# Performance work log

Hardware: AMD Instinct MI355X
Metric: run time of the kernel (lower is better)

## Reference

```python
import jax, jax.numpy as jnp
import numpy as np

SEQ_LEN = 128
EMBED_DIM = 1024
BATCH = 128


def setup_inputs() -> dict:
    key = jax.random.key(0)
    ks = jax.random.split(key, 9)
    d = EMBED_DIM
    s = 0.02
    return {
        "x": jax.random.normal(ks[0], (BATCH, SEQ_LEN * d), dtype=jnp.float32),
        "Wq": jax.random.normal(ks[1], (d, d), dtype=jnp.float32) * s,
        "bq": jax.random.normal(ks[2], (d,), dtype=jnp.float32) * s,
        "Wk": jax.random.normal(ks[3], (d, d), dtype=jnp.float32) * s,
        "bk": jax.random.normal(ks[4], (d,), dtype=jnp.float32) * s,
        "Wv": jax.random.normal(ks[5], (d, d), dtype=jnp.float32) * s,
        "bv": jax.random.normal(ks[6], (d,), dtype=jnp.float32) * s,
        "Wo": jax.random.normal(ks[7], (d, d), dtype=jnp.float32) * s,
        "bo": jax.random.normal(ks[8], (d,), dtype=jnp.float32) * s,
    }


def reference(x, Wq, bq, Wk, bk, Wv, bv, Wo, bo):
    b = x.shape[0]
    d = EMBED_DIM
    xs = x.reshape(b, SEQ_LEN, d)  # [B, S, D]
    # torch Linear: y = x @ W.T + b
    Q = jnp.einsum("bsd,ed->bse", xs, Wq) + bq
    K = jnp.einsum("bsd,ed->bse", xs, Wk) + bk
    V = jnp.einsum("bsd,ed->bse", xs, Wv) + bv
    scores = jnp.einsum("bse,bte->bst", Q, K) / jnp.sqrt(jnp.float32(d))
    weights = jax.nn.softmax(scores, axis=-1)
    attended = jnp.einsum("bst,bte->bse", weights, V)
    out = jnp.einsum("bse,fe->bsf", attended, Wo) + bo
    return out.reshape(b, -1)
```

## Files before the change

kernel.cpp:

```cpp
#include <hip/hip_runtime.h>
#include <hip/hip_bf16.h>

typedef __attribute__((ext_vector_type(8))) __bf16 bf16x8;
typedef __attribute__((ext_vector_type(4))) __bf16 bf16x4;
typedef __attribute__((ext_vector_type(4))) float f32x4;

#define SEQ 128
#define DIM 1024
#define BATCH 128
#define MTOT (BATCH * SEQ)

__device__ __forceinline__ void gload16(const void* g, void* l) {
    __builtin_amdgcn_global_load_lds(
        (const __attribute__((address_space(1))) void*)g,
        (__attribute__((address_space(3))) void*)l, 16, 0, 0);
}

#define BARRIER() do { asm volatile("" ::: "memory"); __builtin_amdgcn_s_barrier(); asm volatile("" ::: "memory"); } while (0)
#define WAITV(N) asm volatile("s_waitcnt vmcnt(" #N ")" ::: "memory")
#define MFMA(a, b, c) __builtin_amdgcn_mfma_f32_16x16x32_bf16(a, b, c, 0, 0, 0)

__global__ void cast_all(const float* __restrict__ x,
                         const float* __restrict__ Wq, const float* __restrict__ Wk,
                         const float* __restrict__ Wv, const float* __restrict__ Wo,
                         __bf16* __restrict__ Xb,
                         __bf16* __restrict__ Wqb, __bf16* __restrict__ Wkb,
                         __bf16* __restrict__ Wvb, __bf16* __restrict__ Wob) {
    const float* src; __bf16* dst; size_t base;
    if (blockIdx.y == 0) {
        src = x; dst = Xb; base = (size_t)blockIdx.x * 2048;
    } else {
        const int j = blockIdx.x;
        if (j >= 2048) return;
        const int w = j >> 9;
        src = (w == 0) ? Wq : (w == 1) ? Wk : (w == 2) ? Wv : Wo;
        dst = (w == 0) ? Wqb : (w == 1) ? Wkb : (w == 2) ? Wvb : Wob;
        base = (size_t)(j & 511) * 2048;
    }
    const size_t i = base + (size_t)threadIdx.x * 8;
    float4 f0 = *reinterpret_cast<const float4*>(src + i);
    float4 f1 = *reinterpret_cast<const float4*>(src + i + 4);
    bf16x8 o;
    o[0] = (__bf16)f0.x; o[1] = (__bf16)f0.y; o[2] = (__bf16)f0.z; o[3] = (__bf16)f0.w;
    o[4] = (__bf16)f1.x; o[5] = (__bf16)f1.y; o[6] = (__bf16)f1.z; o[7] = (__bf16)f1.w;
    *reinterpret_cast<bf16x8*>(dst + i) = o;
}

#define GEMM_TILE_BODY(RB, SB, TS, DOSTAGE, VMSTMT) do { \
    const __bf16* As_ = &lds[RB][wr][0]; \
    const __bf16* Bs_ = &lds[RB][2 + (wc >> 1)][0]; \
    const int bb_ = (wc & 1) * 64; \
    bf16x8 a0 = LDF(As_, 0 * 16 + lr), a1 = LDF(As_, 1 * 16 + lr); \
    bf16x8 a2 = LDF(As_, 2 * 16 + lr), a3 = LDF(As_, 3 * 16 + lr); \
    bf16x8 a4 = LDF(As_, 4 * 16 + lr), a5 = LDF(As_, 5 * 16 + lr); \
    bf16x8 a6 = LDF(As_, 6 * 16 + lr), a7 = LDF(As_, 7 * 16 + lr); \
    bf16x8 b0 = LDF(Bs_, bb_ + 0 * 16 + lr), b1 = LDF(Bs_, bb_ + 1 * 16 + lr); \
    bf16x8 b2 = LDF(Bs_, bb_ + 2 * 16 + lr), b3 = LDF(Bs_, bb_ + 3 * 16 + lr); \
    if (DOSTAGE) { STAGE_A(SB, TS); STAGE_B(SB, TS); } \
    __builtin_amdgcn_s_setprio(1); \
    acc[0][0] = MFMA(a0, b0, acc[0][0]); acc[0][1] = MFMA(a0, b1, acc[0][1]); \
    acc[0][2] = MFMA(a0, b2, acc[0][2]); acc[0][3] = MFMA(a0, b3, acc[0][3]); \
    acc[1][0] = MFMA(a1, b0, acc[1][0]); acc[1][1] = MFMA(a1, b1, acc[1][1]); \
    acc[1][2] = MFMA(a1, b2, acc[1][2]); acc[1][3] = MFMA(a1, b3, acc[1][3]); \
    acc[2][0] = MFMA(a2, b0, acc[2][0]); acc[2][1] = MFMA(a2, b1, acc[2][1]); \
    acc[2][2] = MFMA(a2, b2, acc[2][2]); acc[2][3] = MFMA(a2, b3, acc[2][3]); \
    acc[3][0] = MFMA(a3, b0, acc[3][0]); acc[3][1] = MFMA(a3, b1, acc[3][1]); \
    acc[3][2] = MFMA(a3, b2, acc[3][2]); acc[3][3] = MFMA(a3, b3, acc[3][3]); \
    acc[4][0] = MFMA(a4, b0, acc[4][0]); acc[4][1] = MFMA(a4, b1, acc[4][1]); \
    acc[4][2] = MFMA(a4, b2, acc[4][2]); acc[4][3] = MFMA(a4, b3, acc[4][3]); \
    acc[5][0] = MFMA(a5, b0, acc[5][0]); acc[5][1] = MFMA(a5, b1, acc[5][1]); \
    acc[5][2] = MFMA(a5, b2, acc[5][2]); acc[5][3] = MFMA(a5, b3, acc[5][3]); \
    acc[6][0] = MFMA(a6, b0, acc[6][0]); acc[6][1] = MFMA(a6, b1, acc[6][1]); \
    acc[6][2] = MFMA(a6, b2, acc[6][2]); acc[6][3] = MFMA(a6, b3, acc[6][3]); \
    acc[7][0] = MFMA(a7, b0, acc[7][0]); acc[7][1] = MFMA(a7, b1, acc[7][1]); \
    acc[7][2] = MFMA(a7, b2, acc[7][2]); acc[7][3] = MFMA(a7, b3, acc[7][3]); \
    __builtin_amdgcn_s_setprio(0); \
    VMSTMT; \
    BARRIER(); \
} while (0)

#define GEMM_MAIN_LOOP() do { \
    STAGE_A(0, 0); STAGE_B(0, 0); \
    STAGE_A(1, 1); STAGE_B(1, 1); \
    STAGE_A(2, 2); STAGE_B(2, 2); \
    WAITV(8); \
    BARRIER(); \
    for (int it = 0; it < 7; ++it) { \
        const int t = it * 4; \
        GEMM_TILE_BODY(0, 3, t + 3, 1, WAITV(8)); \
        GEMM_TILE_BODY(1, 0, t + 4, 1, WAITV(8)); \
        GEMM_TILE_BODY(2, 1, t + 5, 1, WAITV(8)); \
        GEMM_TILE_BODY(3, 2, t + 6, 1, WAITV(8)); \
    } \
    GEMM_TILE_BODY(0, 3, 31, 1, WAITV(8));    \
    GEMM_TILE_BODY(1, 0, 0, 0, WAITV(4));     \
    GEMM_TILE_BODY(2, 0, 0, 0, WAITV(0));     \
    GEMM_TILE_BODY(3, 0, 0, 0, (void)0);      \
} while (0)

__global__ __launch_bounds__(512, 1) void gemm_qkv3(const __bf16* __restrict__ A,
        const __bf16* __restrict__ Wqb, const __bf16* __restrict__ Wkb, const __bf16* __restrict__ Wvb,
        const float* __restrict__ bq, const float* __restrict__ bk, const float* __restrict__ bv,
        __bf16* __restrict__ Qo, __bf16* __restrict__ Ko, __bf16* __restrict__ Vt) {
    const int K = 1024;
    __shared__ __bf16 lds[4][4][4096];
    const int tid = threadIdx.x, wave = tid >> 6, lane = tid & 63;
    const int wr = wave >> 2, wc = wave & 3;
    const int lr = lane & 15;
    const int lkb = ((lane >> 4) & 3) * 16;
    const unsigned bid = blockIdx.x;
    const unsigned swz = (bid & 7) * 96 + (bid >> 3);
    const int mt = swz / 12, nt = swz % 12;
    const int m0 = mt * 256;
    const int n0row = (nt & 3) * 256;
    const int mid = nt >> 2;
    const __bf16* Wsel = (mid == 0) ? Wqb : (mid == 1) ? Wkb : Wvb;
    const float*  bsel = (mid == 0) ? bq  : (mid == 1) ? bk  : bv;

    const int rloc = wave * 16 + (lane >> 2);
    const int cbs  = ((((lane & 3) << 4) ^ (((lane >> 3) & 3) << 4)) >> 1);
    const __bf16* pA = A + (size_t)(m0 + rloc) * K + cbs;
    const __bf16* pB = Wsel + (size_t)(n0row + rloc) * K + cbs;
    const int wo = wave * 512;

    f32x4 acc[8][4] = {};

#define LDF(SLOT, R) (*reinterpret_cast<const bf16x8*>( \
        reinterpret_cast<const char*>(SLOT) + (R) * 64 + (lkb ^ ((((R) >> 1) & 3) << 4))))
#define STAGE_A(SB, TS) do { gload16(pA + (TS) * 32, &lds[SB][0][wo]); \
                             gload16(pA + (size_t)128 * 1024 + (TS) * 32, &lds[SB][1][wo]); } while (0)
#define STAGE_B(SB, TS) do { gload16(pB + (TS) * 32, &lds[SB][2][wo]); \
                             gload16(pB + (size_t)128 * 1024 + (TS) * 32, &lds[SB][3][wo]); } while (0)

    GEMM_MAIN_LOOP();

    const int rbase = (lane >> 4) * 4;
    #pragma unroll
    for (int ri = 0; ri < 8; ++ri) {
        #pragma unroll
        for (int j = 0; j < 4; ++j) {
            const int gcl = n0row + wc * 64 + j * 16 + lr;
            const float bvv = bsel[gcl];
            const int grb = m0 + wr * 128 + ri * 16 + rbase;
            if (mid < 2) {
                __bf16* C = (mid == 0) ? Qo : Ko;
                #pragma unroll
                for (int r = 0; r < 4; ++r)
                    C[(size_t)(grb + r) * DIM + gcl] = (__bf16)(acc[ri][j][r] + bvv);
            } else {
                const int b = grb >> 7, s = grb & 127;
                bf16x4 v;
                #pragma unroll
                for (int r = 0; r < 4; ++r) v[r] = (__bf16)(acc[ri][j][r] + bvv);
                *reinterpret_cast<bf16x4*>(&Vt[((size_t)b * DIM + gcl) * SEQ + s]) = v;
            }
        }
    }
#undef STAGE_A
#undef STAGE_B
#undef LDF
}

__global__ __launch_bounds__(512, 1) void gemm256o(const __bf16* __restrict__ A,
                                                   const __bf16* __restrict__ W,
                                                   const float* __restrict__ bias,
                                                   float* __restrict__ Cout) {
    const int K = 1024, N = 1024;
    __shared__ __bf16 lds[4][4][4096];
    const int tid = threadIdx.x, wave = tid >> 6, lane = tid & 63;
    const int wr = wave >> 2, wc = wave & 3;
    const int lr = lane & 15;
    const int lkb = ((lane >> 4) & 3) * 16;
    const int bid = blockIdx.x;
    const int swz = (bid & 7) * 32 + (bid >> 3);
    const int m0 = (swz >> 2) * 256, n0 = (swz & 3) * 256;
    const int rloc = wave * 16 + (lane >> 2);
    const int cbs  = ((((lane & 3) << 4) ^ (((lane >> 3) & 3) << 4)) >> 1);
    const __bf16* pA = A + (size_t)(m0 + rloc) * K + cbs;
    const __bf16* pB = W + (size_t)(n0 + rloc) * K + cbs;
    const int wo = wave * 512;

    f32x4 acc[8][4] = {};

#define LDF(SLOT, R) (*reinterpret_cast<const bf16x8*>( \
        reinterpret_cast<const char*>(SLOT) + (R) * 64 + (lkb ^ ((((R) >> 1) & 3) << 4))))
#define STAGE_A(SB, TS) do { gload16(pA + (TS) * 32, &lds[SB][0][wo]); \
                             gload16(pA + (size_t)128 * 1024 + (TS) * 32, &lds[SB][1][wo]); } while (0)
#define STAGE_B(SB, TS) do { gload16(pB + (TS) * 32, &lds[SB][2][wo]); \
                             gload16(pB + (size_t)128 * 1024 + (TS) * 32, &lds[SB][3][wo]); } while (0)

    GEMM_MAIN_LOOP();

    const int rbase = (lane >> 4) * 4;
    #pragma unroll
    for (int ri = 0; ri < 8; ++ri) {
        #pragma unroll
        for (int j = 0; j < 4; ++j) {
            const int gc  = n0 + wc * 64 + j * 16 + lr;
            const float bv = bias[gc];
            const int grb = m0 + wr * 128 + ri * 16 + rbase;
            #pragma unroll
            for (int r = 0; r < 4; ++r)
                Cout[(size_t)(grb + r) * N + gc] = acc[ri][j][r] + bv;
        }
    }
#undef STAGE_A
#undef STAGE_B
#undef LDF
}

__global__ __launch_bounds__(256) void attn_kernel(const __bf16* __restrict__ Q,
                                                   const __bf16* __restrict__ Km,
                                                   const __bf16* __restrict__ Vt,
                                                   __bf16* __restrict__ Ab) {
    __shared__ __align__(16) char smem[40960];
    float  (*Ssh)[132] = (float(*)[132])(smem);
    __bf16 (*Psh)[136] = (__bf16(*)[136])(smem + 16896);

    const int bid = blockIdx.x;
    const int logical = (bid & 7) * 64 + (bid >> 3);
    const int b = logical >> 2, rt = logical & 3;
    const int tid = threadIdx.x, wave = tid >> 6, lane = tid & 63;
    const int lr = lane & 15, lk = (lane >> 4) * 8, rbase = (lane >> 4) * 4;
    const __bf16* Qb = Q  + ((size_t)b * SEQ + rt * 32) * DIM;
    const __bf16* Kb = Km + (size_t)b * SEQ * DIM;
    const __bf16* Vb = Vt + (size_t)b * DIM * SEQ;

    const int csrc = ((lane & 7) * 16) ^ (((lane >> 3) & 7) << 4);

    f32x4 acc[2][2] = {};
    {
        auto stage_kq = [&](int buf, int c) {
            char* Kd = smem + buf * 20480 + wave * 4096;
            char* Qd = smem + buf * 20480 + 16384 + wave * 1024;
            const char* Ks = (const char*)Kb + (size_t)(wave * 32 + (lane >> 3)) * 2048 + c * 128 + csrc;
            #pragma unroll
            for (int q = 0; q < 4; ++q)
                gload16(Ks + (size_t)q * 8 * 2048, Kd + q * 1024);
            const char* Qs = (const char*)Qb + (size_t)(wave * 8 + (lane >> 3)) * 2048 + c * 128 + csrc;
            gload16(Qs, Qd);
        };
        stage_kq(0, 0);
        WAITV(0);
        BARRIER();
        for (int c = 0; c < 16; ++c) {
            const int rb = c & 1;
            if (c < 15) stage_kq(rb ^ 1, c + 1);
            const char* Kl = smem + rb * 20480;
            const char* Ql = Kl + 16384;
            bf16x8 qf[2][2], kf[2][2];
            #pragma unroll
            for (int i = 0; i < 2; ++i)
                #pragma unroll
                for (int ks = 0; ks < 2; ++ks) {
                    const int r = i * 16 + lr;
                    qf[i][ks] = *reinterpret_cast<const bf16x8*>(
                        Ql + r * 128 + ((ks * 64 + (lane >> 4) * 16) ^ ((r & 7) << 4)));
                }
            #pragma unroll
            for (int j = 0; j < 2; ++j)
                #pragma unroll
                for (int ks = 0; ks < 2; ++ks) {
                    const int r = wave * 32 + j * 16 + lr;
                    kf[j][ks] = *reinterpret_cast<const bf16x8*>(
                        Kl + r * 128 + ((ks * 64 + (lane >> 4) * 16) ^ ((r & 7) << 4)));
                }
            __builtin_amdgcn_s_setprio(1);
            #pragma unroll
            for (int i = 0; i < 2; ++i)
                #pragma unroll
                for (int j = 0; j < 2; ++j)
                    #pragma unroll
                    for (int ks = 0; ks < 2; ++ks)
                        acc[i][j] = MFMA(qf[i][ks], kf[j][ks], acc[i][j]);
            __builtin_amdgcn_s_setprio(0);
            WAITV(0);
            BARRIER();
        }
    }
    const float scale = 0.03125f;
    #pragma unroll
    for (int i = 0; i < 2; ++i)
        #pragma unroll
        for (int j = 0; j < 2; ++j)
            #pragma unroll
            for (int r = 0; r < 4; ++r)
                Ssh[i * 16 + rbase + r][wave * 32 + j * 16 + lr] = acc[i][j][r] * scale;
    __syncthreads();

    {
        const int row = tid >> 3;
        const int c0  = (tid & 7) * 16;
        float4 v0 = *reinterpret_cast<const float4*>(&Ssh[row][c0]);
        float4 v1 = *reinterpret_cast<const float4*>(&Ssh[row][c0 + 4]);
        float4 v2 = *reinterpret_cast<const float4*>(&Ssh[row][c0 + 8]);
        float4 v3 = *reinterpret_cast<const float4*>(&Ssh[row][c0 + 12]);
        float e[16] = {v0.x, v0.y, v0.z, v0.w, v1.x, v1.y, v1.z, v1.w,
                       v2.x, v2.y, v2.z, v2.w, v3.x, v3.y, v3.z, v3.w};
        float mx = e[0];
        #pragma unroll
        for (int u = 1; u < 16; ++u) mx = fmaxf(mx, e[u]);
        mx = fmaxf(mx, __shfl_xor(mx, 1));
        mx = fmaxf(mx, __shfl_xor(mx, 2));
        mx = fmaxf(mx, __shfl_xor(mx, 4));
        float s = 0.f;
        #pragma unroll
        for (int u = 0; u < 16; ++u) { e[u] = __expf(e[u] - mx); s += e[u]; }
        s += __shfl_xor(s, 1);
        s += __shfl_xor(s, 2);
        s += __shfl_xor(s, 4);
        const float inv = 1.f / s;
        bf16x8 p0, p1;
        #pragma unroll
        for (int u = 0; u < 8; ++u) { p0[u] = (__bf16)(e[u] * inv); p1[u] = (__bf16)(e[u + 8] * inv); }
        *reinterpret_cast<bf16x8*>(&Psh[row][c0])     = p0;
        *reinterpret_cast<bf16x8*>(&Psh[row][c0 + 8]) = p1;
    }
    __syncthreads();

    bf16x8 pf[2][4];
    #pragma unroll
    for (int i = 0; i < 2; ++i)
        #pragma unroll
        for (int ks = 0; ks < 4; ++ks)
            pf[i][ks] = *reinterpret_cast<const bf16x8*>(&Psh[i * 16 + lr][ks * 32 + lk]);
    __syncthreads();

    __bf16* Ao = Ab + ((size_t)b * SEQ + rt * 32) * DIM;
    {
        auto stage_v = [&](int buf, int c) {
            char* Vd = smem + buf * 16384 + wave * 4096;
            #pragma unroll
            for (int q = 0; q < 4; ++q) {
                const int rowl = wave * 16 + q * 4 + (lane >> 4);
                const char* Vs = (const char*)Vb + (size_t)(c * 64 + rowl) * 256 +
                                 (((lane & 15) * 16) ^ ((rowl & 7) << 4));
                gload16(Vs, Vd + q * 1024);
            }
        };
        stage_v(0, 0);
        WAITV(0);
        BARRIER();
        for (int c = 0; c < 16; ++c) {
            const int rb = c & 1;
            if (c < 15) stage_v(rb ^ 1, c + 1);
            const char* Vl = smem + rb * 16384;
            f32x4 a2[2] = {};
            const int r = wave * 16 + lr;
            #pragma unroll
            for (int ks = 0; ks < 4; ++ks) {
                bf16x8 vf = *reinterpret_cast<const bf16x8*>(
                    Vl + r * 256 + ((ks * 64 + (lane >> 4) * 16) ^ ((r & 7) << 4)));
                a2[0] = MFMA(pf[0][ks], vf, a2[0]);
                a2[1] = MFMA(pf[1][ks], vf, a2[1]);
            }
            const int n0 = c * 64 + wave * 16;
            #pragma unroll
            for (int i = 0; i < 2; ++i)
                #pragma unroll
                for (int rr = 0; rr < 4; ++rr)
                    Ao[(size_t)(i * 16 + rbase + rr) * DIM + n0 + lr] = (__bf16)a2[i][rr];
            WAITV(8);
            BARRIER();
        }
    }
}

extern "C" void kernel_launch(void* const* d_in, const int* in_sizes, int n_in,
                              void* d_out, int out_size, void* d_ws, size_t ws_size,
                              hipStream_t stream) {
    const float* x  = (const float*)d_in[0];
    const float* Wq = (const float*)d_in[1];
    const float* bq = (const float*)d_in[2];
    const float* Wk = (const float*)d_in[3];
    const float* bk = (const float*)d_in[4];
    const float* Wv = (const float*)d_in[5];
    const float* bv = (const float*)d_in[6];
    const float* Wo = (const float*)d_in[7];
    const float* bo = (const float*)d_in[8];

    char* ws = (char*)d_ws;
    const size_t MB = 1024 * 1024;
    __bf16* Xb  = (__bf16*)(ws);
    __bf16* Wqb = (__bf16*)(ws + 32 * MB);
    __bf16* Wkb = (__bf16*)(ws + 34 * MB);
    __bf16* Wvb = (__bf16*)(ws + 36 * MB);
    __bf16* Wob = (__bf16*)(ws + 38 * MB);
    __bf16* Qb  = (__bf16*)(ws + 40 * MB);
    __bf16* Kb  = (__bf16*)(ws + 72 * MB);
    __bf16* Vt  = (__bf16*)(ws + 104 * MB);
    __bf16* Ab  = Xb;

    cast_all<<<dim3(8192, 2), 256, 0, stream>>>(x, Wq, Wk, Wv, Wo, Xb, Wqb, Wkb, Wvb, Wob);

    gemm_qkv3<<<768, 512, 0, stream>>>(Xb, Wqb, Wkb, Wvb, bq, bk, bv, Qb, Kb, Vt);

    attn_kernel<<<512, 256, 0, stream>>>(Qb, Kb, Vt, Ab);

    gemm256o<<<256, 512, 0, stream>>>(Ab, Wob, bo, (float*)d_out);
}
```

Measured before the change: 187.4 us.

## Double-buffer LDS-to-register fragments to overlap LDS reads with MFMA

Restructures the GEMM main loop so the register fragments for the next K-tile are read from LDS while the MFMAs for the current tile run, using two register fragment sets (f0/f1). Global-to-LDS staging is issued at the start of each step, and the vmcnt wait drops from 8 to 4 so the tile being read next is resident. This aims to hide LDS read latency behind matrix math. In exchange it roughly doubles fragment register usage, which could cause spills, and it tightens the wait and barrier ordering around buffer reuse.

```diff
diff --git a/kernel.cpp b/kernel.cpp
--- a/kernel.cpp
+++ b/kernel.cpp
@@ -46,56 +46,63 @@
     *reinterpret_cast<bf16x8*>(dst + i) = o;
 }
 
-#define GEMM_TILE_BODY(RB, SB, TS, DOSTAGE, VMSTMT) do { \
+
+#define RF(P, RB) do { \
     const __bf16* As_ = &lds[RB][wr][0]; \
     const __bf16* Bs_ = &lds[RB][2 + (wc >> 1)][0]; \
     const int bb_ = (wc & 1) * 64; \
-    bf16x8 a0 = LDF(As_, 0 * 16 + lr), a1 = LDF(As_, 1 * 16 + lr); \
-    bf16x8 a2 = LDF(As_, 2 * 16 + lr), a3 = LDF(As_, 3 * 16 + lr); \
-    bf16x8 a4 = LDF(As_, 4 * 16 + lr), a5 = LDF(As_, 5 * 16 + lr); \
-    bf16x8 a6 = LDF(As_, 6 * 16 + lr), a7 = LDF(As_, 7 * 16 + lr); \
-    bf16x8 b0 = LDF(Bs_, bb_ + 0 * 16 + lr), b1 = LDF(Bs_, bb_ + 1 * 16 + lr); \
-    bf16x8 b2 = LDF(Bs_, bb_ + 2 * 16 + lr), b3 = LDF(Bs_, bb_ + 3 * 16 + lr); \
-    if (DOSTAGE) { STAGE_A(SB, TS); STAGE_B(SB, TS); } \
+    P##a0 = LDF(As_, 0 * 16 + lr); P##a1 = LDF(As_, 1 * 16 + lr); \
+    P##a2 = LDF(As_, 2 * 16 + lr); P##a3 = LDF(As_, 3 * 16 + lr); \
+    P##a4 = LDF(As_, 4 * 16 + lr); P##a5 = LDF(As_, 5 * 16 + lr); \
+    P##a6 = LDF(As_, 6 * 16 + lr); P##a7 = LDF(As_, 7 * 16 + lr); \
+    P##b0 = LDF(Bs_, bb_ + 0 * 16 + lr); P##b1 = LDF(Bs_, bb_ + 1 * 16 + lr); \
+    P##b2 = LDF(Bs_, bb_ + 2 * 16 + lr); P##b3 = LDF(Bs_, bb_ + 3 * 16 + lr); \
+} while (0)
+
+#define MM(P) do { \
     __builtin_amdgcn_s_setprio(1); \
-    acc[0][0] = MFMA(a0, b0, acc[0][0]); acc[0][1] = MFMA(a0, b1, acc[0][1]); \
-    acc[0][2] = MFMA(a0, b2, acc[0][2]); acc[0][3] = MFMA(a0, b3, acc[0][3]); \
-    acc[1][0] = MFMA(a1, b0, acc[1][0]); acc[1][1] = MFMA(a1, b1, acc[1][1]); \
-    acc[1][2] = MFMA(a1, b2, acc[1][2]); acc[1][3] = MFMA(a1, b3, acc[1][3]); \
-    acc[2][0] = MFMA(a2, b0, acc[2][0]); acc[2][1] = MFMA(a2, b1, acc[2][1]); \
-    acc[2][2] = MFMA(a2, b2, acc[2][2]); acc[2][3] = MFMA(a2, b3, acc[2][3]); \
-    acc[3][0] = MFMA(a3, b0, acc[3][0]); acc[3][1] = MFMA(a3, b1, acc[3][1]); \
-    acc[3][2] = MFMA(a3, b2, acc[3][2]); acc[3][3] = MFMA(a3, b3, acc[3][3]); \
-    acc[4][0] = MFMA(a4, b0, acc[4][0]); acc[4][1] = MFMA(a4, b1, acc[4][1]); \
-    acc[4][2] = MFMA(a4, b2, acc[4][2]); acc[4][3] = MFMA(a4, b3, acc[4][3]); \
-    acc[5][0] = MFMA(a5, b0, acc[5][0]); acc[5][1] = MFMA(a5, b1, acc[5][1]); \
-    acc[5][2] = MFMA(a5, b2, acc[5][2]); acc[5][3] = MFMA(a5, b3, acc[5][3]); \
-    acc[6][0] = MFMA(a6, b0, acc[6][0]); acc[6][1] = MFMA(a6, b1, acc[6][1]); \
-    acc[6][2] = MFMA(a6, b2, acc[6][2]); acc[6][3] = MFMA(a6, b3, acc[6][3]); \
-    acc[7][0] = MFMA(a7, b0, acc[7][0]); acc[7][1] = MFMA(a7, b1, acc[7][1]); \
-    acc[7][2] = MFMA(a7, b2, acc[7][2]); acc[7][3] = MFMA(a7, b3, acc[7][3]); \
+    acc[0][0] = MFMA(P##a0, P##b0, acc[0][0]); acc[0][1] = MFMA(P##a0, P##b1, acc[0][1]); \
+    acc[0][2] = MFMA(P##a0, P##b2, acc[0][2]); acc[0][3] = MFMA(P##a0, P##b3, acc[0][3]); \
+    acc[1][0] = MFMA(P##a1, P##b0, acc[1][0]); acc[1][1] = MFMA(P##a1, P##b1, acc[1][1]); \
+    acc[1][2] = MFMA(P##a1, P##b2, acc[1][2]); acc[1][3] = MFMA(P##a1, P##b3, acc[1][3]); \
+    acc[2][0] = MFMA(P##a2, P##b0, acc[2][0]); acc[2][1] = MFMA(P##a2, P##b1, acc[2][1]); \
+    acc[2][2] = MFMA(P##a2, P##b2, acc[2][2]); acc[2][3] = MFMA(P##a2, P##b3, acc[2][3]); \
+    acc[3][0] = MFMA(P##a3, P##b0, acc[3][0]); acc[3][1] = MFMA(P##a3, P##b1, acc[3][1]); \
+    acc[3][2] = MFMA(P##a3, P##b2, acc[3][2]); acc[3][3] = MFMA(P##a3, P##b3, acc[3][3]); \
+    acc[4][0] = MFMA(P##a4, P##b0, acc[4][0]); acc[4][1] = MFMA(P##a4, P##b1, acc[4][1]); \
+    acc[4][2] = MFMA(P##a4, P##b2, acc[4][2]); acc[4][3] = MFMA(P##a4, P##b3, acc[4][3]); \
+    acc[5][0] = MFMA(P##a5, P##b0, acc[5][0]); acc[5][1] = MFMA(P##a5, P##b1, acc[5][1]); \
+    acc[5][2] = MFMA(P##a5, P##b2, acc[5][2]); acc[5][3] = MFMA(P##a5, P##b3, acc[5][3]); \
+    acc[6][0] = MFMA(P##a6, P##b0, acc[6][0]); acc[6][1] = MFMA(P##a6, P##b1, acc[6][1]); \
+    acc[6][2] = MFMA(P##a6, P##b2, acc[6][2]); acc[6][3] = MFMA(P##a6, P##b3, acc[6][3]); \
+    acc[7][0] = MFMA(P##a7, P##b0, acc[7][0]); acc[7][1] = MFMA(P##a7, P##b1, acc[7][1]); \
+    acc[7][2] = MFMA(P##a7, P##b2, acc[7][2]); acc[7][3] = MFMA(P##a7, P##b3, acc[7][3]); \
     __builtin_amdgcn_s_setprio(0); \
-    VMSTMT; \
-    BARRIER(); \
 } while (0)
 
-#define GEMM_MAIN_LOOP() do { \
+#define DECL_FRAGS \
+    bf16x8 f0a0, f0a1, f0a2, f0a3, f0a4, f0a5, f0a6, f0a7, f0b0, f0b1, f0b2, f0b3; \
+    bf16x8 f1a0, f1a1, f1a2, f1a3, f1a4, f1a5, f1a6, f1a7, f1b0, f1b1, f1b2, f1b3;
+
+#define GEMM_PIPE_LOOP() do { \
     STAGE_A(0, 0); STAGE_B(0, 0); \
     STAGE_A(1, 1); STAGE_B(1, 1); \
     STAGE_A(2, 2); STAGE_B(2, 2); \
-    WAITV(8); \
+    WAITV(4);       \
     BARRIER(); \
+    RF(f0, 0); \
     for (int it = 0; it < 7; ++it) { \
         const int t = it * 4; \
-        GEMM_TILE_BODY(0, 3, t + 3, 1, WAITV(8)); \
-        GEMM_TILE_BODY(1, 0, t + 4, 1, WAITV(8)); \
-        GEMM_TILE_BODY(2, 1, t + 5, 1, WAITV(8)); \
-        GEMM_TILE_BODY(3, 2, t + 6, 1, WAITV(8)); \
+        STAGE_A(3, t + 3); STAGE_B(3, t + 3); RF(f1, 1); MM(f0); WAITV(4); BARRIER(); \
+        STAGE_A(0, t + 4); STAGE_B(0, t + 4); RF(f0, 2); MM(f1); WAITV(4); BARRIER(); \
+        STAGE_A(1, t + 5); STAGE_B(1, t + 5); RF(f1, 3); MM(f0); WAITV(4); BARRIER(); \
+        STAGE_A(2, t + 6); STAGE_B(2, t + 6); RF(f0, 0); MM(f1); WAITV(4); BARRIER(); \
     } \
-    GEMM_TILE_BODY(0, 3, 31, 1, WAITV(8));    \
-    GEMM_TILE_BODY(1, 0, 0, 0, WAITV(4));     \
-    GEMM_TILE_BODY(2, 0, 0, 0, WAITV(0));     \
-    GEMM_TILE_BODY(3, 0, 0, 0, (void)0);      \
+     \
+    STAGE_A(3, 31); STAGE_B(3, 31); RF(f1, 1); MM(f0); WAITV(4); BARRIER();   \
+    RF(f0, 2); MM(f1); WAITV(0); BARRIER();                                   \
+    RF(f1, 3); MM(f0); BARRIER();                                             \
+    MM(f1);                                                                   \
 } while (0)
 
 __global__ __launch_bounds__(512, 1) void gemm_qkv3(const __bf16* __restrict__ A,
@@ -124,6 +131,7 @@
     const int wo = wave * 512;
 
     f32x4 acc[8][4] = {};
+    DECL_FRAGS
 
 #define LDF(SLOT, R) (*reinterpret_cast<const bf16x8*>( \
         reinterpret_cast<const char*>(SLOT) + (R) * 64 + (lkb ^ ((((R) >> 1) & 3) << 4))))
@@ -132,7 +140,7 @@
 #define STAGE_B(SB, TS) do { gload16(pB + (TS) * 32, &lds[SB][2][wo]); \
                              gload16(pB + (size_t)128 * 1024 + (TS) * 32, &lds[SB][3][wo]); } while (0)
 
-    GEMM_MAIN_LOOP();
+    GEMM_PIPE_LOOP();
 
     const int rbase = (lane >> 4) * 4;
     #pragma unroll
@@ -181,6 +189,7 @@
     const int wo = wave * 512;
 
     f32x4 acc[8][4] = {};
+    DECL_FRAGS
 
 #define LDF(SLOT, R) (*reinterpret_cast<const bf16x8*>( \
         reinterpret_cast<const char*>(SLOT) + (R) * 64 + (lkb ^ ((((R) >> 1) & 3) << 4))))
@@ -189,7 +198,7 @@
 #define STAGE_B(SB, TS) do { gload16(pB + (TS) * 32, &lds[SB][2][wo]); \
                              gload16(pB + (size_t)128 * 1024 + (TS) * 32, &lds[SB][3][wo]); } while (0)
 
-    GEMM_MAIN_LOOP();
+    GEMM_PIPE_LOOP();
 
     const int rbase = (lane >> 4) * 4;
     #pragma unroll
```

Result: slower. 211.4 us (+12.8%).

## Fuse fp32-to-bf16 cast of x into QKV GEMM A-tile staging

Applied to the files above, without the earlier changes.

Drops the separate cast pass over the large activation tensor x. The QKV GEMM now reads fp32 x directly, converts it to bf16 in registers and writes it to LDS with ordinary stores; only the weights are still pre-cast. The waitcnt values are adjusted to count only the remaining async B loads. This saves a full read and write of x, but the A loads become synchronous register loads that can stall the pipelined main loop, and the GEMM fetches twice the bytes per A tile across its repeated tile reads.

```diff
diff --git a/kernel.cpp b/kernel.cpp
--- a/kernel.cpp
+++ b/kernel.cpp
@@ -20,24 +20,15 @@
 #define WAITV(N) asm volatile("s_waitcnt vmcnt(" #N ")" ::: "memory")
 #define MFMA(a, b, c) __builtin_amdgcn_mfma_f32_16x16x32_bf16(a, b, c, 0, 0, 0)
 
-__global__ void cast_all(const float* __restrict__ x,
-                         const float* __restrict__ Wq, const float* __restrict__ Wk,
-                         const float* __restrict__ Wv, const float* __restrict__ Wo,
-                         __bf16* __restrict__ Xb,
-                         __bf16* __restrict__ Wqb, __bf16* __restrict__ Wkb,
-                         __bf16* __restrict__ Wvb, __bf16* __restrict__ Wob) {
-    const float* src; __bf16* dst; size_t base;
-    if (blockIdx.y == 0) {
-        src = x; dst = Xb; base = (size_t)blockIdx.x * 2048;
-    } else {
-        const int j = blockIdx.x;
-        if (j >= 2048) return;
-        const int w = j >> 9;
-        src = (w == 0) ? Wq : (w == 1) ? Wk : (w == 2) ? Wv : Wo;
-        dst = (w == 0) ? Wqb : (w == 1) ? Wkb : (w == 2) ? Wvb : Wob;
-        base = (size_t)(j & 511) * 2048;
-    }
-    const size_t i = base + (size_t)threadIdx.x * 8;
+__global__ void cast_w(const float* __restrict__ Wq, const float* __restrict__ Wk,
+                       const float* __restrict__ Wv, const float* __restrict__ Wo,
+                       __bf16* __restrict__ Wqb, __bf16* __restrict__ Wkb,
+                       __bf16* __restrict__ Wvb, __bf16* __restrict__ Wob) {
+    const int j = blockIdx.x;
+    const int w = j >> 9;
+    const float* src = (w == 0) ? Wq : (w == 1) ? Wk : (w == 2) ? Wv : Wo;
+    __bf16* dst = (w == 0) ? Wqb : (w == 1) ? Wkb : (w == 2) ? Wvb : Wob;
+    const size_t i = (size_t)(j & 511) * 2048 + (size_t)threadIdx.x * 8;
     float4 f0 = *reinterpret_cast<const float4*>(src + i);
     float4 f1 = *reinterpret_cast<const float4*>(src + i + 4);
     bf16x8 o;
@@ -79,26 +70,7 @@
     BARRIER(); \
 } while (0)
 
-#define GEMM_MAIN_LOOP() do { \
-    STAGE_A(0, 0); STAGE_B(0, 0); \
-    STAGE_A(1, 1); STAGE_B(1, 1); \
-    STAGE_A(2, 2); STAGE_B(2, 2); \
-    WAITV(8); \
-    BARRIER(); \
-    for (int it = 0; it < 7; ++it) { \
-        const int t = it * 4; \
-        GEMM_TILE_BODY(0, 3, t + 3, 1, WAITV(8)); \
-        GEMM_TILE_BODY(1, 0, t + 4, 1, WAITV(8)); \
-        GEMM_TILE_BODY(2, 1, t + 5, 1, WAITV(8)); \
-        GEMM_TILE_BODY(3, 2, t + 6, 1, WAITV(8)); \
-    } \
-    GEMM_TILE_BODY(0, 3, 31, 1, WAITV(8));    \
-    GEMM_TILE_BODY(1, 0, 0, 0, WAITV(4));     \
-    GEMM_TILE_BODY(2, 0, 0, 0, WAITV(0));     \
-    GEMM_TILE_BODY(3, 0, 0, 0, (void)0);      \
-} while (0)
-
-__global__ __launch_bounds__(512, 1) void gemm_qkv3(const __bf16* __restrict__ A,
+__global__ __launch_bounds__(512, 1) void gemm_qkv3(const float* __restrict__ X,
         const __bf16* __restrict__ Wqb, const __bf16* __restrict__ Wkb, const __bf16* __restrict__ Wvb,
         const float* __restrict__ bq, const float* __restrict__ bk, const float* __restrict__ bv,
         __bf16* __restrict__ Qo, __bf16* __restrict__ Ko, __bf16* __restrict__ Vt) {
@@ -119,20 +91,48 @@
 
     const int rloc = wave * 16 + (lane >> 2);
     const int cbs  = ((((lane & 3) << 4) ^ (((lane >> 3) & 3) << 4)) >> 1);
-    const __bf16* pA = A + (size_t)(m0 + rloc) * K + cbs;
-    const __bf16* pB = Wsel + (size_t)(n0row + rloc) * K + cbs;
+    const float*  pXf = X + (size_t)(m0 + rloc) * K + cbs;
+    const __bf16* pB  = Wsel + (size_t)(n0row + rloc) * K + cbs;
     const int wo = wave * 512;
 
     f32x4 acc[8][4] = {};
 
 #define LDF(SLOT, R) (*reinterpret_cast<const bf16x8*>( \
         reinterpret_cast<const char*>(SLOT) + (R) * 64 + (lkb ^ ((((R) >> 1) & 3) << 4))))
-#define STAGE_A(SB, TS) do { gload16(pA + (TS) * 32, &lds[SB][0][wo]); \
-                             gload16(pA + (size_t)128 * 1024 + (TS) * 32, &lds[SB][1][wo]); } while (0)
+#define STAGE_A(SB, TS) do { \
+    const float* s_ = pXf + (TS) * 32; \
+    float4 u0_ = *reinterpret_cast<const float4*>(s_); \
+    float4 u1_ = *reinterpret_cast<const float4*>(s_ + 4); \
+    float4 v0_ = *reinterpret_cast<const float4*>(s_ + (size_t)128 * 1024); \
+    float4 v1_ = *reinterpret_cast<const float4*>(s_ + (size_t)128 * 1024 + 4); \
+    bf16x8 w0_, w1_; \
+    w0_[0] = (__bf16)u0_.x; w0_[1] = (__bf16)u0_.y; w0_[2] = (__bf16)u0_.z; w0_[3] = (__bf16)u0_.w; \
+    w0_[4] = (__bf16)u1_.x; w0_[5] = (__bf16)u1_.y; w0_[6] = (__bf16)u1_.z; w0_[7] = (__bf16)u1_.w; \
+    w1_[0] = (__bf16)v0_.x; w1_[1] = (__bf16)v0_.y; w1_[2] = (__bf16)v0_.z; w1_[3] = (__bf16)v0_.w; \
+    w1_[4] = (__bf16)v1_.x; w1_[5] = (__bf16)v1_.y; w1_[6] = (__bf16)v1_.z; w1_[7] = (__bf16)v1_.w; \
+    *reinterpret_cast<bf16x8*>(reinterpret_cast<char*>(&lds[SB][0][wo]) + lane * 16) = w0_; \
+    *reinterpret_cast<bf16x8*>(reinterpret_cast<char*>(&lds[SB][1][wo]) + lane * 16) = w1_; \
+} while (0)
 #define STAGE_B(SB, TS) do { gload16(pB + (TS) * 32, &lds[SB][2][wo]); \
                              gload16(pB + (size_t)128 * 1024 + (TS) * 32, &lds[SB][3][wo]); } while (0)
 
-    GEMM_MAIN_LOOP();
+    STAGE_A(0, 0); STAGE_B(0, 0);
+    STAGE_A(1, 1); STAGE_B(1, 1);
+    STAGE_A(2, 2); STAGE_B(2, 2);
+    WAITV(4);
+    BARRIER();
+
+    for (int it = 0; it < 7; ++it) {
+        const int t = it * 4;
+        GEMM_TILE_BODY(0, 3, t + 3, 1, WAITV(4));
+        GEMM_TILE_BODY(1, 0, t + 4, 1, WAITV(4));
+        GEMM_TILE_BODY(2, 1, t + 5, 1, WAITV(4));
+        GEMM_TILE_BODY(3, 2, t + 6, 1, WAITV(4));
+    }
+    GEMM_TILE_BODY(0, 3, 31, 1, WAITV(4));
+    GEMM_TILE_BODY(1, 0, 0, 0, WAITV(2));
+    GEMM_TILE_BODY(2, 0, 0, 0, WAITV(0));
+    GEMM_TILE_BODY(3, 0, 0, 0, (void)0);
 
     const int rbase = (lane >> 4) * 4;
     #pragma unroll
@@ -189,7 +189,23 @@
 #define STAGE_B(SB, TS) do { gload16(pB + (TS) * 32, &lds[SB][2][wo]); \
                              gload16(pB + (size_t)128 * 1024 + (TS) * 32, &lds[SB][3][wo]); } while (0)
 
-    GEMM_MAIN_LOOP();
+    STAGE_A(0, 0); STAGE_B(0, 0);
+    STAGE_A(1, 1); STAGE_B(1, 1);
+    STAGE_A(2, 2); STAGE_B(2, 2);
+    WAITV(8);
+    BARRIER();
+
+    for (int it = 0; it < 7; ++it) {
+        const int t = it * 4;
+        GEMM_TILE_BODY(0, 3, t + 3, 1, WAITV(8));
+        GEMM_TILE_BODY(1, 0, t + 4, 1, WAITV(8));
+        GEMM_TILE_BODY(2, 1, t + 5, 1, WAITV(8));
+        GEMM_TILE_BODY(3, 2, t + 6, 1, WAITV(8));
+    }
+    GEMM_TILE_BODY(0, 3, 31, 1, WAITV(8));
+    GEMM_TILE_BODY(1, 0, 0, 0, WAITV(4));
+    GEMM_TILE_BODY(2, 0, 0, 0, WAITV(0));
+    GEMM_TILE_BODY(3, 0, 0, 0, (void)0);
 
     const int rbase = (lane >> 4) * 4;
     #pragma unroll
@@ -381,7 +397,7 @@
 
     char* ws = (char*)d_ws;
     const size_t MB = 1024 * 1024;
-    __bf16* Xb  = (__bf16*)(ws);
+    __bf16* Ab  = (__bf16*)(ws);
     __bf16* Wqb = (__bf16*)(ws + 32 * MB);
     __bf16* Wkb = (__bf16*)(ws + 34 * MB);
     __bf16* Wvb = (__bf16*)(ws + 36 * MB);
@@ -389,11 +405,10 @@
     __bf16* Qb  = (__bf16*)(ws + 40 * MB);
     __bf16* Kb  = (__bf16*)(ws + 72 * MB);
     __bf16* Vt  = (__bf16*)(ws + 104 * MB);
-    __bf16* Ab  = Xb;
-
-    cast_all<<<dim3(8192, 2), 256, 0, stream>>>(x, Wq, Wk, Wv, Wo, Xb, Wqb, Wkb, Wvb, Wob);
-
-    gemm_qkv3<<<768, 512, 0, stream>>>(Xb, Wqb, Wkb, Wvb, bq, bk, bv, Qb, Kb, Vt);
+
+    cast_w<<<2048, 256, 0, stream>>>(Wq, Wk, Wv, Wo, Wqb, Wkb, Wvb, Wob);
+
+    gemm_qkv3<<<768, 512, 0, stream>>>(x, Wqb, Wkb, Wvb, bq, bk, bv, Qb, Kb, Vt);
 
     attn_kernel<<<512, 256, 0, stream>>>(Qb, Kb, Vt, Ab);
 
```

After: 242.2 us. 1.29x slower.

## Load GEMM weight fragments directly from global into registers, bypassing LDS

Applied to the files above, without the earlier changes.

Both GEMM kernels stop staging the weight (B) tile through LDS. Each wave now loads its B fragments straight from global memory into registers every k-step, and LDS keeps only the A tile, which halves shared memory use. The intent is to cut LDS traffic and async-copy bookkeeping. The cost is that global loads now sit directly on the MFMA critical path with no prefetch, and the weights are read redundantly by the two wave rows. The vmcnt wait counts are adjusted, but synchronous register loads interact with those waits and may add stalls.

```diff
diff --git a/kernel.cpp b/kernel.cpp
--- a/kernel.cpp
+++ b/kernel.cpp
@@ -46,17 +46,17 @@
     *reinterpret_cast<bf16x8*>(dst + i) = o;
 }
 
-#define GEMM_TILE_BODY(RB, SB, TS, DOSTAGE, VMSTMT) do { \
+#define GEMM_TILE_BODY(RB, SB, TB, TSG, DOSTAGE, VMSTMT) do { \
+    bf16x8 b0 = *reinterpret_cast<const bf16x8*>(Bg + (TB) * 32 + 0 * 16384); \
+    bf16x8 b1 = *reinterpret_cast<const bf16x8*>(Bg + (TB) * 32 + 1 * 16384); \
+    bf16x8 b2 = *reinterpret_cast<const bf16x8*>(Bg + (TB) * 32 + 2 * 16384); \
+    bf16x8 b3 = *reinterpret_cast<const bf16x8*>(Bg + (TB) * 32 + 3 * 16384); \
     const __bf16* As_ = &lds[RB][wr][0]; \
-    const __bf16* Bs_ = &lds[RB][2 + (wc >> 1)][0]; \
-    const int bb_ = (wc & 1) * 64; \
     bf16x8 a0 = LDF(As_, 0 * 16 + lr), a1 = LDF(As_, 1 * 16 + lr); \
     bf16x8 a2 = LDF(As_, 2 * 16 + lr), a3 = LDF(As_, 3 * 16 + lr); \
     bf16x8 a4 = LDF(As_, 4 * 16 + lr), a5 = LDF(As_, 5 * 16 + lr); \
     bf16x8 a6 = LDF(As_, 6 * 16 + lr), a7 = LDF(As_, 7 * 16 + lr); \
-    bf16x8 b0 = LDF(Bs_, bb_ + 0 * 16 + lr), b1 = LDF(Bs_, bb_ + 1 * 16 + lr); \
-    bf16x8 b2 = LDF(Bs_, bb_ + 2 * 16 + lr), b3 = LDF(Bs_, bb_ + 3 * 16 + lr); \
-    if (DOSTAGE) { STAGE_A(SB, TS); STAGE_B(SB, TS); } \
+    if (DOSTAGE) STAGE_A(SB, TSG); \
     __builtin_amdgcn_s_setprio(1); \
     acc[0][0] = MFMA(a0, b0, acc[0][0]); acc[0][1] = MFMA(a0, b1, acc[0][1]); \
     acc[0][2] = MFMA(a0, b2, acc[0][2]); acc[0][3] = MFMA(a0, b3, acc[0][3]); \
@@ -80,22 +80,20 @@
 } while (0)
 
 #define GEMM_MAIN_LOOP() do { \
-    STAGE_A(0, 0); STAGE_B(0, 0); \
-    STAGE_A(1, 1); STAGE_B(1, 1); \
-    STAGE_A(2, 2); STAGE_B(2, 2); \
-    WAITV(8); \
+    STAGE_A(0, 0); STAGE_A(1, 1); STAGE_A(2, 2); \
+    WAITV(4); \
     BARRIER(); \
     for (int it = 0; it < 7; ++it) { \
         const int t = it * 4; \
-        GEMM_TILE_BODY(0, 3, t + 3, 1, WAITV(8)); \
-        GEMM_TILE_BODY(1, 0, t + 4, 1, WAITV(8)); \
-        GEMM_TILE_BODY(2, 1, t + 5, 1, WAITV(8)); \
-        GEMM_TILE_BODY(3, 2, t + 6, 1, WAITV(8)); \
+        GEMM_TILE_BODY(0, 3, t + 0, t + 3, 1, WAITV(4)); \
+        GEMM_TILE_BODY(1, 0, t + 1, t + 4, 1, WAITV(4)); \
+        GEMM_TILE_BODY(2, 1, t + 2, t + 5, 1, WAITV(4)); \
+        GEMM_TILE_BODY(3, 2, t + 3, t + 6, 1, WAITV(4)); \
     } \
-    GEMM_TILE_BODY(0, 3, 31, 1, WAITV(8));    \
-    GEMM_TILE_BODY(1, 0, 0, 0, WAITV(4));     \
-    GEMM_TILE_BODY(2, 0, 0, 0, WAITV(0));     \
-    GEMM_TILE_BODY(3, 0, 0, 0, (void)0);      \
+    GEMM_TILE_BODY(0, 3, 28, 31, 1, WAITV(4)); \
+    GEMM_TILE_BODY(1, 0, 29, 0, 0, WAITV(2)); \
+    GEMM_TILE_BODY(2, 0, 30, 0, 0, WAITV(0)); \
+    GEMM_TILE_BODY(3, 0, 31, 0, 0, (void)0); \
 } while (0)
 
 __global__ __launch_bounds__(512, 1) void gemm_qkv3(const __bf16* __restrict__ A,
@@ -103,7 +101,7 @@
         const float* __restrict__ bq, const float* __restrict__ bk, const float* __restrict__ bv,
         __bf16* __restrict__ Qo, __bf16* __restrict__ Ko, __bf16* __restrict__ Vt) {
     const int K = 1024;
-    __shared__ __bf16 lds[4][4][4096];
+    __shared__ __bf16 lds[4][2][4096];
     const int tid = threadIdx.x, wave = tid >> 6, lane = tid & 63;
     const int wr = wave >> 2, wc = wave & 3;
     const int lr = lane & 15;
@@ -120,7 +118,7 @@
     const int rloc = wave * 16 + (lane >> 2);
     const int cbs  = ((((lane & 3) << 4) ^ (((lane >> 3) & 3) << 4)) >> 1);
     const __bf16* pA = A + (size_t)(m0 + rloc) * K + cbs;
-    const __bf16* pB = Wsel + (size_t)(n0row + rloc) * K + cbs;
+    const __bf16* Bg = Wsel + (size_t)(n0row + wc * 64 + (lane & 15)) * K + ((lane >> 4) & 3) * 8;
     const int wo = wave * 512;
 
     f32x4 acc[8][4] = {};
@@ -129,8 +127,6 @@
         reinterpret_cast<const char*>(SLOT) + (R) * 64 + (lkb ^ ((((R) >> 1) & 3) << 4))))
 #define STAGE_A(SB, TS) do { gload16(pA + (TS) * 32, &lds[SB][0][wo]); \
                              gload16(pA + (size_t)128 * 1024 + (TS) * 32, &lds[SB][1][wo]); } while (0)
-#define STAGE_B(SB, TS) do { gload16(pB + (TS) * 32, &lds[SB][2][wo]); \
-                             gload16(pB + (size_t)128 * 1024 + (TS) * 32, &lds[SB][3][wo]); } while (0)
 
     GEMM_MAIN_LOOP();
 
@@ -157,7 +153,6 @@
         }
     }
 #undef STAGE_A
-#undef STAGE_B
 #undef LDF
 }
 
@@ -166,7 +161,7 @@
                                                    const float* __restrict__ bias,
                                                    float* __restrict__ Cout) {
     const int K = 1024, N = 1024;
-    __shared__ __bf16 lds[4][4][4096];
+    __shared__ __bf16 lds[4][2][4096];
     const int tid = threadIdx.x, wave = tid >> 6, lane = tid & 63;
     const int wr = wave >> 2, wc = wave & 3;
     const int lr = lane & 15;
@@ -177,7 +172,7 @@
     const int rloc = wave * 16 + (lane >> 2);
     const int cbs  = ((((lane & 3) << 4) ^ (((lane >> 3) & 3) << 4)) >> 1);
     const __bf16* pA = A + (size_t)(m0 + rloc) * K + cbs;
-    const __bf16* pB = W + (size_t)(n0 + rloc) * K + cbs;
+    const __bf16* Bg = W + (size_t)(n0 + wc * 64 + (lane & 15)) * K + ((lane >> 4) & 3) * 8;
     const int wo = wave * 512;
 
     f32x4 acc[8][4] = {};
@@ -186,8 +181,6 @@
         reinterpret_cast<const char*>(SLOT) + (R) * 64 + (lkb ^ ((((R) >> 1) & 3) << 4))))
 #define STAGE_A(SB, TS) do { gload16(pA + (TS) * 32, &lds[SB][0][wo]); \
                              gload16(pA + (size_t)128 * 1024 + (TS) * 32, &lds[SB][1][wo]); } while (0)
-#define STAGE_B(SB, TS) do { gload16(pB + (TS) * 32, &lds[SB][2][wo]); \
-                             gload16(pB + (size_t)128 * 1024 + (TS) * 32, &lds[SB][3][wo]); } while (0)
 
     GEMM_MAIN_LOOP();
 
@@ -205,7 +198,6 @@
         }
     }
 #undef STAGE_A
-#undef STAGE_B
 #undef LDF
 }
 
```

Measured after the change: 269.6 us. 1.44x slower.
